# Optimization experiments

Measured on AMD Instinct MI355X. Metric: run time of the kernel, lower is better.

Reference implementation:

```python
import jax, jax.numpy as jnp
import numpy as np

NUM_NODES = 50000
NUM_EDGES = 1600000
IN_DIM = 128
OUT_DIM = 128
BATCH = 2


def setup_inputs() -> dict:
    key = jax.random.key(0)
    k1, k2, k3 = jax.random.split(key, 3)
    inputs = jax.random.normal(k1, (BATCH, NUM_NODES, IN_DIM), dtype=jnp.float32)
    W = jax.random.normal(k2, (IN_DIM, OUT_DIM), dtype=jnp.float32) * 0.02
    bias = jnp.zeros((1, 1, OUT_DIM), dtype=jnp.float32)
    adjacency_list = jax.random.randint(k3, (NUM_EDGES, 2), 0, NUM_NODES, dtype=jnp.int32)
    return {"inputs": inputs, "W": W, "bias": bias, "adjacency_list": adjacency_list}


def reference(inputs, W, bias, adjacency_list):
    # inputs: (B, N, Din); adjacency_list: (E, 2) with [:,0]=src, [:,1]=dst
    N = inputs.shape[1]
    src = adjacency_list[:, 0]
    dst = adjacency_list[:, 1]
    # symmetric-normalization weights, as computed in __init__
    deg = jnp.bincount(src, length=N)                      # (N,)
    node_w = jnp.sqrt(1.0 / (deg.astype(inputs.dtype) + 1.0))  # (N,)
    edge_w = node_w[src] * node_w[dst]                     # (E,)
    # dense projection (no activation: activation=None)
    x = jnp.einsum('bnd,do->bno', inputs, W)               # (B, N, Dout)
    # gather by edge source, scale by edge weight
    gathered = x[:, src, :] * edge_w[None, :, None]        # (B, E, Dout)
    # scatter-add into destination nodes (unsorted_segment_sum)
    agg = jnp.zeros_like(x).at[:, dst, :].add(gathered)    # (B, N, Dout)
    # self-loop term + aggregated neighbors + bias
    out = (node_w ** 2)[None, :, None] * x + agg + bias
    return out
```

## Files before the change

### kernel.cpp

```cpp
#include <hip/hip_runtime.h>
#include <hip/hip_bf16.h>


#define NN 50000
#define EE 1600000
#define DD 128
#define BB 2
#define NB 128
#define CHUNK 12500
#define HS 50000
#define HW4 (HS / 4)
#define SLOTS 96

typedef __attribute__((ext_vector_type(8))) short short8;
typedef __attribute__((ext_vector_type(8))) unsigned short ushort8v;
typedef __attribute__((ext_vector_type(4))) float floatx4;
typedef __attribute__((ext_vector_type(2))) float floatx2;
typedef __attribute__((ext_vector_type(4))) unsigned int uintx4;

__device__ inline unsigned short f2bf(float f) {
    unsigned u = __float_as_uint(f);
    unsigned r = u + 0x7fffu + ((u >> 16) & 1u);
    return (unsigned short)(r >> 16);
}
__device__ inline float bf2f(unsigned short h) {
    return __uint_as_float(((unsigned)h) << 16);
}

__global__ __launch_bounds__(1024) void phist_kernel(const int4* __restrict__ adj2,
                                                     unsigned int* __restrict__ histD32,
                                                     unsigned int* __restrict__ histS32,
                                                     unsigned char* __restrict__ rank) {
    __shared__ unsigned int h[HW4];
    int b = blockIdx.x;
    int p0 = b * (CHUNK / 2);

    for (int i = threadIdx.x; i < HW4; i += 1024) h[i] = 0;
    __syncthreads();
    if (blockIdx.y == 0) {
        for (int i = threadIdx.x; i < CHUNK / 2; i += 1024) {
            int4 two = adj2[p0 + i];
            unsigned ka = (unsigned)two.y, kb = (unsigned)two.w;
            unsigned sha = (ka & 3u) << 3, shb = (kb & 3u) << 3;
            unsigned olda = atomicAdd(&h[ka >> 2], 1u << sha);
            unsigned oldb = atomicAdd(&h[kb >> 2], 1u << shb);
            unsigned r0 = (olda >> sha) & 0xffu;
            unsigned r1 = (oldb >> shb) & 0xffu;
            int e = b * CHUNK + 2 * i;
            *(unsigned short*)(rank + e) = (unsigned short)(r0 | (r1 << 8));
        }
        __syncthreads();
        for (int i = threadIdx.x; i < HW4; i += 1024) histD32[(size_t)b * HW4 + i] = h[i];
    } else {
        for (int i = threadIdx.x; i < CHUNK / 2; i += 1024) {
            int4 two = adj2[p0 + i];
            unsigned ka = (unsigned)two.x, kb = (unsigned)two.z;
            atomicAdd(&h[ka >> 2], 1u << ((ka & 3u) << 3));
            atomicAdd(&h[kb >> 2], 1u << ((kb & 3u) << 3));
        }
        __syncthreads();
        for (int i = threadIdx.x; i < HW4; i += 1024) histS32[(size_t)b * HW4 + i] = h[i];
    }
}

__global__ __launch_bounds__(256) void reduce_hist_kernel(unsigned char* __restrict__ histD,
                                                          const unsigned char* __restrict__ histS,
                                                          unsigned char* __restrict__ deg8,
                                                          float* __restrict__ node_w) {
    int k = blockIdx.x * 256 + threadIdx.x;
    if (k >= NN) return;
    unsigned run = 0;
#pragma unroll 8
    for (int b = 0; b < NB; ++b) {
        size_t idx = (size_t)b * HS + k;
        unsigned c = histD[idx];
        histD[idx] = (unsigned char)run;
        run += c;
    }
    deg8[k] = (unsigned char)run;

    unsigned s = 0;
#pragma unroll 8
    for (int b = 0; b < NB; ++b) s += histS[(size_t)b * HS + k];
    node_w[k] = rsqrtf((float)s + 1.0f);
}

__global__ __launch_bounds__(256) void scatter_kernel(const int4* __restrict__ adj2,
                                                      const unsigned short* __restrict__ rank16,
                                                      const unsigned char* __restrict__ histD,
                                                      unsigned short* __restrict__ csr_src) {
    int i = blockIdx.x * blockDim.x + threadIdx.x;
    int4 two = adj2[i];
    unsigned rr = rank16[i];
    int e = 2 * i;
    int b = e / CHUNK;
    int posA = two.y * SLOTS + (int)histD[(size_t)b * HS + two.y] + (int)(rr & 0xffu);
    int posB = two.w * SLOTS + (int)histD[(size_t)b * HS + two.w] + (int)(rr >> 8);
    csr_src[posA] = (unsigned short)two.x;
    csr_src[posB] = (unsigned short)two.z;
}

#define WT_STRIDE 136
__global__ __launch_bounds__(1024) void gemm_mfma_kernel(const float* __restrict__ in,
                                                         const float* __restrict__ W,
                                                         const float* __restrict__ node_w,
                                                         unsigned short* __restrict__ y,
                                                         int total_rows) {
    __shared__ unsigned short wt[128 * WT_STRIDE];
    for (int i = threadIdx.x; i < 128 * 128; i += 1024) {
        int d = i >> 7, o = i & 127;
        wt[o * WT_STRIDE + d] = f2bf(W[i]);
    }
    __syncthreads();

    int wave = threadIdx.x >> 6;
    int lane = threadIdx.x & 63;
    int m = lane & 15;
    int quad = lane >> 4;
    int rt = (blockIdx.x * 16 + wave) * 16;
    if (rt >= total_rows) return;

    short8 a[4];
    const float* arow = in + (size_t)(rt + m) * 128;
#pragma unroll
    for (int kt = 0; kt < 4; ++kt) {
        int k0 = kt * 32 + quad * 8;
        float4 f0 = *(const float4*)(arow + k0);
        float4 f1 = *(const float4*)(arow + k0 + 4);
        short8 av;
        av[0] = (short)f2bf(f0.x); av[1] = (short)f2bf(f0.y);
        av[2] = (short)f2bf(f0.z); av[3] = (short)f2bf(f0.w);
        av[4] = (short)f2bf(f1.x); av[5] = (short)f2bf(f1.y);
        av[6] = (short)f2bf(f1.z); av[7] = (short)f2bf(f1.w);
        a[kt] = av;
    }

    float nw[4];
#pragma unroll
    for (int r = 0; r < 4; ++r) {
        int row = rt + quad * 4 + r;
        int n = row - (row >= NN ? NN : 0);
        nw[r] = node_w[n];
    }

#pragma unroll
    for (int ct = 0; ct < 8; ++ct) {
        floatx4 acc = {0.f, 0.f, 0.f, 0.f};
#pragma unroll
        for (int kt = 0; kt < 4; ++kt) {
            const short8* bp =
                (const short8*)&wt[(ct * 16 + m) * WT_STRIDE + kt * 32 + quad * 8];
            acc = __builtin_amdgcn_mfma_f32_16x16x32_bf16(a[kt], *bp, acc, 0, 0, 0);
        }
        int col = ct * 16 + m;
#pragma unroll
        for (int r = 0; r < 4; ++r) {
            int row = rt + quad * 4 + r;
            y[(size_t)row * 128 + col] = f2bf(nw[r] * acc[r]);
        }
    }
}

__global__ __launch_bounds__(256, 8) void aggregate_kernel(
    const unsigned short* __restrict__ yb, const unsigned short* __restrict__ csr_src,
    const unsigned char* __restrict__ deg8, const float* __restrict__ node_w,
    const float* __restrict__ bias, float* __restrict__ out) {
    int wave = threadIdx.x >> 6;
    int lane = threadIdx.x & 63;
    unsigned blk = blockIdx.x;
    int xcd = (int)(blk & 7u);
    int bg = xcd >> 2;
    int nbid = (int)(blk >> 3) * 4 + (xcd & 3);
    int n = nbid * 4 + wave;

    int g = lane >> 4;
    int c8 = lane & 15;
    int c16 = c8 * 16;
    const char* ybase = (const char*)yb + (size_t)bg * (NN * 128 * 2);

    int start = n * SLOTS;
    int cnt = __builtin_amdgcn_readfirstlane((int)deg8[n]);

    floatx2 acc2[4];
#pragma unroll
    for (int k = 0; k < 4; ++k) acc2[k] = (floatx2){0.f, 0.f};

#define ACC16(LD)                                                       \
    {                                                                   \
        _Pragma("unroll") for (int d = 0; d < 4; ++d) {                 \
            floatx2 v2;                                                 \
            v2.x = __uint_as_float((LD)[d] << 16);                      \
            v2.y = __uint_as_float((LD)[d] & 0xffff0000u);              \
            acc2[d] += v2;                                              \
        }                                                               \
    }

    for (int base = 0; base < cnt; base += 64) {
        int mm = cnt - base; if (mm > 64) mm = 64;
        int v = (lane < mm) ? (int)csr_src[start + base + lane] : 0x7fffffff;
#pragma unroll
        for (int k = 2; k <= 32; k <<= 1) {
#pragma unroll
            for (int j = k >> 1; j > 0; j >>= 1) {
                int other = __shfl_xor(v, j);
                bool lower = (lane & j) == 0;
                bool up = (lane & k) == 0;
                int mn = other < v ? other : v;
                int mx = other < v ? v : other;
                v = up ? (lower ? mn : mx) : (lower ? mx : mn);
            }
        }
        if (mm > 32) {
#pragma unroll
            for (int j = 32; j > 0; j >>= 1) {
                int other = __shfl_xor(v, j);
                bool lower = (lane & j) == 0;
                int mn = other < v ? other : v;
                int mx = other < v ? v : other;
                v = lower ? mn : mx;
            }
        }
        int sv = v << 8;
        int j = 0;
        for (; j + 16 <= mm; j += 16) {
            int o0 = __shfl(sv, j + g) + c16;
            int o1 = __shfl(sv, j + 4 + g) + c16;
            int o2 = __shfl(sv, j + 8 + g) + c16;
            int o3 = __shfl(sv, j + 12 + g) + c16;
            uintx4 ld0 = *(const uintx4*)(ybase + (unsigned)o0);
            uintx4 ld1 = *(const uintx4*)(ybase + (unsigned)o1);
            uintx4 ld2 = *(const uintx4*)(ybase + (unsigned)o2);
            uintx4 ld3 = *(const uintx4*)(ybase + (unsigned)o3);
            ACC16(ld0) ACC16(ld1) ACC16(ld2) ACC16(ld3)
        }
        for (; j + 8 <= mm; j += 8) {
            int o0 = __shfl(sv, j + g) + c16;
            int o1 = __shfl(sv, j + 4 + g) + c16;
            uintx4 ld0 = *(const uintx4*)(ybase + (unsigned)o0);
            uintx4 ld1 = *(const uintx4*)(ybase + (unsigned)o1);
            ACC16(ld0) ACC16(ld1)
        }
        if (j < mm) {
            int i0 = j + g, i1 = j + 4 + g;
            int o0 = __shfl(sv, i0 < mm ? i0 : 0) + c16;
            int o1 = __shfl(sv, i1 < mm ? i1 : 0) + c16;
            if (i0 < mm) {
                uintx4 ld0 = *(const uintx4*)(ybase + (unsigned)o0);
                ACC16(ld0)
            }
            if (i1 < mm) {
                uintx4 ld1 = *(const uintx4*)(ybase + (unsigned)o1);
                ACC16(ld1)
            }
        }
    }
#undef ACC16

#pragma unroll
    for (int k = 0; k < 4; ++k) {
        acc2[k].x += __shfl_xor(acc2[k].x, 16);
        acc2[k].x += __shfl_xor(acc2[k].x, 32);
        acc2[k].y += __shfl_xor(acc2[k].y, 16);
        acc2[k].y += __shfl_xor(acc2[k].y, 32);
    }

    if (g == 0) {
        float nw = node_w[n];
        const unsigned short* ys = yb + (size_t)bg * (NN * 128) + (size_t)n * 128 + c8 * 8;
        ushort8v yv = *(const ushort8v*)ys;
        floatx4 o0, o1;
        const float* bp = bias + c8 * 8;
        o0.x = nw * (acc2[0].x + bf2f((unsigned short)yv[0])) + bp[0];
        o0.y = nw * (acc2[0].y + bf2f((unsigned short)yv[1])) + bp[1];
        o0.z = nw * (acc2[1].x + bf2f((unsigned short)yv[2])) + bp[2];
        o0.w = nw * (acc2[1].y + bf2f((unsigned short)yv[3])) + bp[3];
        o1.x = nw * (acc2[2].x + bf2f((unsigned short)yv[4])) + bp[4];
        o1.y = nw * (acc2[2].y + bf2f((unsigned short)yv[5])) + bp[5];
        o1.z = nw * (acc2[3].x + bf2f((unsigned short)yv[6])) + bp[6];
        o1.w = nw * (acc2[3].y + bf2f((unsigned short)yv[7])) + bp[7];
        float* op = out + ((size_t)bg * NN + n) * 128 + c8 * 8;
        __builtin_nontemporal_store(o0, (floatx4*)op);
        __builtin_nontemporal_store(o1, (floatx4*)(op + 4));
    }
}

extern "C" void kernel_launch(void* const* d_in, const int* in_sizes, int n_in,
                              void* d_out, int out_size, void* d_ws, size_t ws_size,
                              hipStream_t stream) {
    const float* inputs = (const float*)d_in[0];
    const float* W      = (const float*)d_in[1];
    const float* bias   = (const float*)d_in[2];
    const int*   adj    = (const int*)d_in[3];
    float* out = (float*)d_out;

    const int total_rows = BB * NN;

    char* ws = (char*)d_ws;
    size_t off = 0;
    unsigned short* y = (unsigned short*)(ws + off);
    off += (size_t)BB * NN * DD * sizeof(unsigned short);
    unsigned char* histD = (unsigned char*)(ws + off);
    off += (size_t)NB * HS;
    unsigned short* csr_src = (unsigned short*)(ws + off);
    unsigned char* histS = (unsigned char*)(ws + off);
    off += (size_t)NN * SLOTS * sizeof(unsigned short);
    unsigned char* rank = (unsigned char*)(ws + off);
    off += (size_t)EE;
    unsigned char* deg8 = (unsigned char*)(ws + off);
    off += (size_t)((NN + 255) & ~255);
    float* node_w = (float*)(ws + off);  off += (size_t)NN * sizeof(float);

    dim3 hgrid(NB, 2);
    phist_kernel<<<hgrid, 1024, 0, stream>>>((const int4*)adj, (unsigned int*)histD,
                                             (unsigned int*)histS, rank);
    reduce_hist_kernel<<<(NN + 255) / 256, 256, 0, stream>>>(histD, histS, deg8, node_w);
    scatter_kernel<<<EE / 2 / 256, 256, 0, stream>>>((const int4*)adj,
                                                     (const unsigned short*)rank, histD,
                                                     csr_src);
    gemm_mfma_kernel<<<(total_rows + 255) / 256, 1024, 0, stream>>>(inputs, W, node_w, y,
                                                                    total_rows);
    aggregate_kernel<<<NN / 4 * BB, 256, 0, stream>>>(y, csr_src, deg8, node_w, bias, out);
}
```

Before: 254.7 us.

## Replace histogram-based CSR build with global atomic slot counters

Drops the three-kernel CSR construction (per-chunk shared-memory histograms with ranks, prefix reduction, and a scatter) and replaces it with one memset plus a single kernel. That kernel uses global atomicAdd on per-node destination counters to claim a slot and also counts source degrees. Node weights are now computed inline from the source counts in the GEMM and aggregate kernels instead of being stored in a node_w array. This removes two kernel launches and the histogram traffic, but it puts 3.2M contended global atomics on the critical path and makes the edge order inside each node's CSR row nondeterministic, which changes the float summation order.

```diff
diff --git a/kernel.cpp b/kernel.cpp
--- a/kernel.cpp
+++ b/kernel.cpp
@@ -6,10 +6,6 @@
 #define EE 1600000
 #define DD 128
 #define BB 2
-#define NB 128
-#define CHUNK 12500
-#define HS 50000
-#define HW4 (HS / 4)
 #define SLOTS 96
 
 typedef __attribute__((ext_vector_type(8))) short short8;
@@ -27,83 +23,23 @@
     return __uint_as_float(((unsigned)h) << 16);
 }
 
-__global__ __launch_bounds__(1024) void phist_kernel(const int4* __restrict__ adj2,
-                                                     unsigned int* __restrict__ histD32,
-                                                     unsigned int* __restrict__ histS32,
-                                                     unsigned char* __restrict__ rank) {
-    __shared__ unsigned int h[HW4];
-    int b = blockIdx.x;
-    int p0 = b * (CHUNK / 2);
-
-    for (int i = threadIdx.x; i < HW4; i += 1024) h[i] = 0;
-    __syncthreads();
-    if (blockIdx.y == 0) {
-        for (int i = threadIdx.x; i < CHUNK / 2; i += 1024) {
-            int4 two = adj2[p0 + i];
-            unsigned ka = (unsigned)two.y, kb = (unsigned)two.w;
-            unsigned sha = (ka & 3u) << 3, shb = (kb & 3u) << 3;
-            unsigned olda = atomicAdd(&h[ka >> 2], 1u << sha);
-            unsigned oldb = atomicAdd(&h[kb >> 2], 1u << shb);
-            unsigned r0 = (olda >> sha) & 0xffu;
-            unsigned r1 = (oldb >> shb) & 0xffu;
-            int e = b * CHUNK + 2 * i;
-            *(unsigned short*)(rank + e) = (unsigned short)(r0 | (r1 << 8));
-        }
-        __syncthreads();
-        for (int i = threadIdx.x; i < HW4; i += 1024) histD32[(size_t)b * HW4 + i] = h[i];
-    } else {
-        for (int i = threadIdx.x; i < CHUNK / 2; i += 1024) {
-            int4 two = adj2[p0 + i];
-            unsigned ka = (unsigned)two.x, kb = (unsigned)two.z;
-            atomicAdd(&h[ka >> 2], 1u << ((ka & 3u) << 3));
-            atomicAdd(&h[kb >> 2], 1u << ((kb & 3u) << 3));
-        }
-        __syncthreads();
-        for (int i = threadIdx.x; i < HW4; i += 1024) histS32[(size_t)b * HW4 + i] = h[i];
-    }
-}
-
-__global__ __launch_bounds__(256) void reduce_hist_kernel(unsigned char* __restrict__ histD,
-                                                          const unsigned char* __restrict__ histS,
-                                                          unsigned char* __restrict__ deg8,
-                                                          float* __restrict__ node_w) {
-    int k = blockIdx.x * 256 + threadIdx.x;
-    if (k >= NN) return;
-    unsigned run = 0;
-#pragma unroll 8
-    for (int b = 0; b < NB; ++b) {
-        size_t idx = (size_t)b * HS + k;
-        unsigned c = histD[idx];
-        histD[idx] = (unsigned char)run;
-        run += c;
-    }
-    deg8[k] = (unsigned char)run;
-
-    unsigned s = 0;
-#pragma unroll 8
-    for (int b = 0; b < NB; ++b) s += histS[(size_t)b * HS + k];
-    node_w[k] = rsqrtf((float)s + 1.0f);
-}
-
-__global__ __launch_bounds__(256) void scatter_kernel(const int4* __restrict__ adj2,
-                                                      const unsigned short* __restrict__ rank16,
-                                                      const unsigned char* __restrict__ histD,
-                                                      unsigned short* __restrict__ csr_src) {
+__global__ __launch_bounds__(256) void scatter_atomic_kernel(
+    const int4* __restrict__ adj2, unsigned int* __restrict__ cntD,
+    unsigned int* __restrict__ cntS, unsigned short* __restrict__ csr_src) {
     int i = blockIdx.x * blockDim.x + threadIdx.x;
     int4 two = adj2[i];
-    unsigned rr = rank16[i];
-    int e = 2 * i;
-    int b = e / CHUNK;
-    int posA = two.y * SLOTS + (int)histD[(size_t)b * HS + two.y] + (int)(rr & 0xffu);
-    int posB = two.w * SLOTS + (int)histD[(size_t)b * HS + two.w] + (int)(rr >> 8);
-    csr_src[posA] = (unsigned short)two.x;
-    csr_src[posB] = (unsigned short)two.z;
+    unsigned pA = atomicAdd(&cntD[two.y], 1u);
+    csr_src[two.y * SLOTS + pA] = (unsigned short)two.x;
+    atomicAdd(&cntS[two.x], 1u);
+    unsigned pB = atomicAdd(&cntD[two.w], 1u);
+    csr_src[two.w * SLOTS + pB] = (unsigned short)two.z;
+    atomicAdd(&cntS[two.z], 1u);
 }
 
 #define WT_STRIDE 136
 __global__ __launch_bounds__(1024) void gemm_mfma_kernel(const float* __restrict__ in,
                                                          const float* __restrict__ W,
-                                                         const float* __restrict__ node_w,
+                                                         const unsigned int* __restrict__ cntS,
                                                          unsigned short* __restrict__ y,
                                                          int total_rows) {
     __shared__ unsigned short wt[128 * WT_STRIDE];
@@ -140,7 +76,7 @@
     for (int r = 0; r < 4; ++r) {
         int row = rt + quad * 4 + r;
         int n = row - (row >= NN ? NN : 0);
-        nw[r] = node_w[n];
+        nw[r] = rsqrtf((float)cntS[n] + 1.0f);
     }
 
 #pragma unroll
@@ -163,7 +99,7 @@
 
 __global__ __launch_bounds__(256, 8) void aggregate_kernel(
     const unsigned short* __restrict__ yb, const unsigned short* __restrict__ csr_src,
-    const unsigned char* __restrict__ deg8, const float* __restrict__ node_w,
+    const unsigned int* __restrict__ cntD, const unsigned int* __restrict__ cntS,
     const float* __restrict__ bias, float* __restrict__ out) {
     int wave = threadIdx.x >> 6;
     int lane = threadIdx.x & 63;
@@ -179,7 +115,7 @@
     const char* ybase = (const char*)yb + (size_t)bg * (NN * 128 * 2);
 
     int start = n * SLOTS;
-    int cnt = __builtin_amdgcn_readfirstlane((int)deg8[n]);
+    int cnt = __builtin_amdgcn_readfirstlane((int)cntD[n]);
 
     floatx2 acc2[4];
 #pragma unroll
@@ -265,7 +201,7 @@
     }
 
     if (g == 0) {
-        float nw = node_w[n];
+        float nw = rsqrtf((float)cntS[n] + 1.0f);
         const unsigned short* ys = yb + (size_t)bg * (NN * 128) + (size_t)n * 128 + c8 * 8;
         ushort8v yv = *(const ushort8v*)ys;
         floatx4 o0, o1;
@@ -299,25 +235,17 @@
     size_t off = 0;
     unsigned short* y = (unsigned short*)(ws + off);
     off += (size_t)BB * NN * DD * sizeof(unsigned short);
-    unsigned char* histD = (unsigned char*)(ws + off);
-    off += (size_t)NB * HS;
     unsigned short* csr_src = (unsigned short*)(ws + off);
-    unsigned char* histS = (unsigned char*)(ws + off);
     off += (size_t)NN * SLOTS * sizeof(unsigned short);
-    unsigned char* rank = (unsigned char*)(ws + off);
-    off += (size_t)EE;
-    unsigned char* deg8 = (unsigned char*)(ws + off);
-    off += (size_t)((NN + 255) & ~255);
-    float* node_w = (float*)(ws + off);  off += (size_t)NN * sizeof(float);
-
-    dim3 hgrid(NB, 2);
-    phist_kernel<<<hgrid, 1024, 0, stream>>>((const int4*)adj, (unsigned int*)histD,
-                                             (unsigned int*)histS, rank);
-    reduce_hist_kernel<<<(NN + 255) / 256, 256, 0, stream>>>(histD, histS, deg8, node_w);
-    scatter_kernel<<<EE / 2 / 256, 256, 0, stream>>>((const int4*)adj,
-                                                     (const unsigned short*)rank, histD,
-                                                     csr_src);
-    gemm_mfma_kernel<<<(total_rows + 255) / 256, 1024, 0, stream>>>(inputs, W, node_w, y,
+    unsigned int* cnt = (unsigned int*)(ws + off);
+    off += (size_t)2 * NN * sizeof(unsigned int);
+    unsigned int* cntD = cnt;
+    unsigned int* cntS = cnt + NN;
+
+    hipMemsetAsync(cnt, 0, (size_t)2 * NN * sizeof(unsigned int), stream);
+    scatter_atomic_kernel<<<EE / 2 / 256, 256, 0, stream>>>((const int4*)adj, cntD, cntS,
+                                                            csr_src);
+    gemm_mfma_kernel<<<(total_rows + 255) / 256, 1024, 0, stream>>>(inputs, W, cntS, y,
                                                                     total_rows);
-    aggregate_kernel<<<NN / 4 * BB, 256, 0, stream>>>(y, csr_src, deg8, node_w, bias, out);
-}
+    aggregate_kernel<<<NN / 4 * BB, 256, 0, stream>>>(y, csr_src, cntD, cntS, bias, out);
+}
```

Result: slower. 356.1 us (+39.8%).
